# Performance work log

Hardware: AMD Instinct MI355X
Metric: run time of the kernel (lower is better)

Reference implementation:

```python
import jax, jax.numpy as jnp
import numpy as np

B, S, K, N = 4, 2048, 4096, 11008
GROUP_SIZE = 128
NUM_GROUPS = K // GROUP_SIZE  # 32


def setup_inputs() -> dict:
    key = jax.random.key(0)
    k1, k2, k3, k4, k5 = jax.random.split(key, 5)
    x = jax.random.normal(k1, (B, S, K), dtype=jnp.float32)
    # sensitivity-sorted column order is a permutation of [0, K)
    col_indices = jax.random.permutation(k2, K).astype(jnp.int32)
    # packed uint8 nibbles stored as int32 in [0, 256)
    w_packed = jax.random.randint(k3, (K // 2, N), 0, 256, dtype=jnp.int32)
    # per-group, per-output-column dequant scales (positive, small)
    scales = (jax.random.uniform(k4, (NUM_GROUPS, N), dtype=jnp.float32) + 0.05) * 0.01
    bias = jax.random.normal(k5, (N,), dtype=jnp.float32) * 0.01
    return {"x": x, "col_indices": col_indices, "w_packed": w_packed,
            "scales": scales, "bias": bias}


def _dequant_weight(w_packed, scales):
    # unpack int4 nibbles: low nibble -> even k, high nibble -> odd k
    low = (w_packed & 15) - 8          # [K//2, N]
    high = ((w_packed >> 4) & 15) - 8  # [K//2, N]
    w_int = jnp.stack([low, high], axis=1).reshape(K, N)  # interleaved [K, N]
    # per-group dequant: scale index = k // group_size
    w = w_int.astype(scales.dtype).reshape(NUM_GROUPS, GROUP_SIZE, N)
    w = w * scales[:, None, :]
    return w.reshape(K, N)


def reference(x, col_indices, w_packed, scales, bias):
    orig_shape = x.shape
    xm = x.reshape(-1, K)                     # [M, K]
    xg = jnp.take(xm, col_indices, axis=1)    # column-reorder gather [M, K]
    w = _dequant_weight(w_packed, scales)     # [K, N]
    out = jnp.einsum('mk,kn->mn', xg, w)      # fp32 accumulate
    out = out + bias
    return out.reshape(orig_shape[0], orig_shape[1], N)
```

## Files before the change

kernel.cpp:

```cpp
#include <hip/hip_runtime.h>
#include <hip/hip_bf16.h>
#include <stdint.h>

#define M_DIM 8192
#define K_DIM 4096
#define N_DIM 11008
#define NT32  128

typedef __attribute__((ext_vector_type(8))) short bf16x8;
typedef __attribute__((ext_vector_type(4))) float f32x4;
typedef __attribute__((ext_vector_type(4))) unsigned int uint4v;

__device__ __forceinline__ unsigned short f2bf(float f) {
    __hip_bfloat16 h = __float2bfloat16(f);
    return __builtin_bit_cast(unsigned short, h);
}

__device__ __forceinline__ void gload_lds16(const unsigned short* g, unsigned short* l) {
    __builtin_amdgcn_global_load_lds(
        (const __attribute__((address_space(1))) void*)g,
        (__attribute__((address_space(3))) void*)l,
        16, 0, 0);
}

__device__ __forceinline__ unsigned lds_addr(const unsigned short* p) {
    return (unsigned)(uintptr_t)(const __attribute__((address_space(3))) unsigned short*)p;
}

#define DSRI(dst, a, OFF) asm volatile("ds_read_b128 %0, %1 offset:%2" \
    : "=v"(dst) : "v"(a), "n"(OFF) : "memory")

#define LGKM(N) do { \
    asm volatile("s_waitcnt lgkmcnt(" #N ")" ::: "memory"); \
    __builtin_amdgcn_sched_barrier(0); \
} while (0)
#define BAR() do { __builtin_amdgcn_s_barrier(); asm volatile("" ::: "memory"); } while (0)

__global__ void permute_x_kernel(const float* __restrict__ x,
                                 const int* __restrict__ ci,
                                 unsigned short* __restrict__ xg) {
    int idx = blockIdx.x * 256 + threadIdx.x;
    int64_t base = (int64_t)idx * 4;
    int m = (int)(base >> 12);
    int k = (int)(base & 4095);
    const float* xrow = x + ((int64_t)m << 12);
    int4 c4 = *reinterpret_cast<const int4*>(ci + k);
    ushort4 o;
    o.x = f2bf(xrow[c4.x]);
    o.y = f2bf(xrow[c4.y]);
    o.z = f2bf(xrow[c4.z]);
    o.w = f2bf(xrow[c4.w]);
    *reinterpret_cast<ushort4*>(xg + base) = o;
}

__global__ void dequant_w_kernel(const int* __restrict__ wp,
                                 const float* __restrict__ scales,
                                 unsigned short* __restrict__ wT) {
    __shared__ unsigned short tile[64][65];
    int n0 = blockIdx.x * 64;
    int k0 = blockIdx.y * 64;
    int g = k0 >> 7;
    int t = threadIdx.x;
    int col = t & 63;
    int r0 = t >> 6;
    float s = scales[(int64_t)g * N_DIM + n0 + col];
    int pr0 = k0 >> 1;
#pragma unroll
    for (int i = 0; i < 8; ++i) {
        int row = r0 + i * 4;
        int p = wp[(int64_t)(pr0 + row) * N_DIM + n0 + col];
        tile[2 * row][col]     = f2bf((float)((p & 15) - 8) * s);
        tile[2 * row + 1][col] = f2bf((float)(((p >> 4) & 15) - 8) * s);
    }
    __syncthreads();
    int nl = t >> 2;
    int kk0 = (t & 3) << 4;
    unsigned short vals[16];
#pragma unroll
    for (int j = 0; j < 16; ++j) vals[j] = tile[kk0 + j][nl];
    uint4v* dst = reinterpret_cast<uint4v*>(wT + (int64_t)(n0 + nl) * K_DIM + k0 + kk0);
    dst[0] = *reinterpret_cast<const uint4v*>(&vals[0]);
    dst[1] = *reinterpret_cast<const uint4v*>(&vals[8]);
}


template <int BUF>
__device__ __forceinline__ void read_RA(bf16x8 (&a)[4], bf16x8 (&b)[4],
                                        unsigned aA01, unsigned aA2,
                                        unsigned bB01, unsigned bB2) {
    const unsigned ad = (BUF < 2) ? aA01 : aA2;
    const unsigned bd = (BUF < 2) ? bB01 : bB2;
    constexpr int bo = (BUF < 2) ? BUF * 32768 : 0;
    DSRI(a[0], ad, bo + 0);
    DSRI(a[1], ad, bo + 1024);
    DSRI(a[2], ad, bo + 2048);
    DSRI(a[3], ad, bo + 3072);
    DSRI(b[0], bd, bo + 0);
    DSRI(b[1], bd, bo + 1024);
    DSRI(b[2], bd, bo + 2048);
    DSRI(b[3], bd, bo + 3072);
}

template <int BUF>
__device__ __forceinline__ void read_RB(bf16x8 (&a2)[4], unsigned aA01, unsigned aA2) {
    const unsigned ad = (BUF < 2) ? aA01 : aA2;
    constexpr int bo = (BUF < 2) ? BUF * 32768 : 0;
    DSRI(a2[0], ad, bo + 4096);
    DSRI(a2[1], ad, bo + 5120);
    DSRI(a2[2], ad, bo + 6144);
    DSRI(a2[3], ad, bo + 7168);
}

template <int MB>
__device__ __forceinline__ void mfma4(f32x4 (&acc)[8][4], const bf16x8 (&av)[4],
                                      const bf16x8 (&bv)[4]) {
    __builtin_amdgcn_s_setprio(1);
#pragma unroll
    for (int m = 0; m < 4; ++m)
#pragma unroll
        for (int n = 0; n < 4; ++n)
            acc[MB + m][n] = __builtin_amdgcn_mfma_f32_16x16x32_bf16(
                av[m], bv[n], acc[MB + m][n], 0, 0, 0);
    __builtin_amdgcn_s_setprio(0);
}

template <int DBUF, int ISB>
__device__ __forceinline__ void stage2(const unsigned short* p0, const unsigned short* p1,
                                       int t, unsigned short* lds, int wLds) {
    const unsigned short* s0 = p0 + t * 32;
    const unsigned short* s1 = p1 + t * 32;
    unsigned short* d = lds + DBUF * 16384 + ISB * 8192 + wLds;
    gload_lds16(s0, d);
    gload_lds16(s1, d + 512);
}

#define PH_TILE(B, BN, BS, CA_, CB_, NA_, NB_, tt)                        \
    do {                                                                  \
        read_RB<B>(a2, aA01, aA2);                                        \
        stage2<BS, 0>(pA0, pA1, (tt), lds, wLds);                         \
        LGKM(4);                                                          \
        mfma4<0>(acc, CA_, CB_);                                          \
        asm volatile("s_waitcnt vmcnt(2)" ::: "memory");                  \
        BAR();                                                            \
        read_RA<BN>(NA_, NB_, aA01, aA2, bB01, bB2);                      \
        stage2<BS, 1>(pB0, pB1, (tt), lds, wLds);                         \
        LGKM(8);                                                          \
        mfma4<4>(acc, a2, CB_);                                           \
        BAR();                                                            \
    } while (0)

__global__ __launch_bounds__(512, 2)
void gemm_kernel(const unsigned short* __restrict__ A,
                 const unsigned short* __restrict__ BT,
                 const float* __restrict__ bias,
                 float* __restrict__ C) {
    __shared__ unsigned short lds[49152];

    constexpr int NT = N_DIM / 256;
    int wg = blockIdx.x, nwg = gridDim.x;
    int q = nwg >> 3, r = nwg & 7;
    int xcd = wg & 7, li = wg >> 3;
    int swz = (xcd < r ? xcd * (q + 1) : r * (q + 1) + (xcd - r) * q) + li;
    int by = swz / NT, bx = swz - by * NT;
    int brow = by << 8, bcol = bx << 8;

    int t = threadIdx.x;
    int lane = t & 63, w = t >> 6;
    int wr = w >> 2, wc = w & 3;
    int fr = lane & 15, fq = lane >> 4;

    const unsigned xr = (unsigned)((fr & 6) << 3);
    const int riw = lane >> 2;
    const int s8 = ((lane & 3) ^ ((lane >> 3) & 3)) << 3;
    const int w32 = w * 32, wLds = w * 1024;

    const unsigned ldsB = lds_addr(lds);
    const unsigned aA01 = ldsB + ((unsigned)((wr * 128 + fr) * 64 + fq * 16) ^ xr);
    const unsigned bB01 = ldsB + 16384u + ((unsigned)((wc * 64 + fr) * 64 + fq * 16) ^ xr);
    const unsigned aA2 = aA01 + 65536;
    const unsigned bB2 = bB01 + 65536;

    const unsigned short* pA0 = A + (int64_t)(brow + w32 + riw) * K_DIM + s8;
    const unsigned short* pA1 = pA0 + 16 * K_DIM;
    const unsigned short* pB0 = BT + (int64_t)(bcol + w32 + riw) * K_DIM + s8;
    const unsigned short* pB1 = pB0 + 16 * K_DIM;

    f32x4 acc[8][4];
#pragma unroll
    for (int m = 0; m < 8; ++m)
#pragma unroll
        for (int n = 0; n < 4; ++n) acc[m][n] = (f32x4){0.f, 0.f, 0.f, 0.f};

    bf16x8 aX[4], bX[4], aY[4], bY[4], a2[4];

    stage2<0, 0>(pA0, pA1, 0, lds, wLds);
    stage2<0, 1>(pB0, pB1, 0, lds, wLds);
    stage2<1, 0>(pA0, pA1, 1, lds, wLds);
    stage2<1, 1>(pB0, pB1, 1, lds, wLds);
    asm volatile("s_waitcnt vmcnt(4)" ::: "memory");
    BAR();
    read_RA<0>(aX, bX, aA01, aA2, bB01, bB2);

#pragma unroll 1
    for (int body = 0; body < 21; ++body) {
        const int t2 = body * 6 + 2;
        PH_TILE(0, 1, 2, aX, bX, aY, bY, t2);
        PH_TILE(1, 2, 0, aY, bY, aX, bX, t2 + 1);
        PH_TILE(2, 0, 1, aX, bX, aY, bY, t2 + 2);
        PH_TILE(0, 1, 2, aY, bY, aX, bX, t2 + 3);
        PH_TILE(1, 2, 0, aX, bX, aY, bY, t2 + 4);
        PH_TILE(2, 0, 1, aY, bY, aX, bX, t2 + 5);
    }

    read_RB<0>(a2, aA01, aA2);
    LGKM(4);
    mfma4<0>(acc, aX, bX);
    asm volatile("s_waitcnt vmcnt(0)" ::: "memory");
    BAR();
    read_RA<1>(aY, bY, aA01, aA2, bB01, bB2);
    LGKM(8);
    mfma4<4>(acc, a2, bX);
    BAR();
    read_RB<1>(a2, aA01, aA2);
    LGKM(4);
    mfma4<0>(acc, aY, bY);
    LGKM(0);
    mfma4<4>(acc, a2, bY);

    int orow0 = brow + wr * 128 + fq * 4;
    int ocol0 = bcol + wc * 64 + fr;
#pragma unroll
    for (int n = 0; n < 4; ++n) {
        int col = ocol0 + n * 16;
        float bval = bias[col];
#pragma unroll
        for (int m = 0; m < 8; ++m) {
            int row = orow0 + m * 16;
            float* cp = C + (int64_t)row * N_DIM + col;
#pragma unroll
            for (int j = 0; j < 4; ++j) {
                cp[(int64_t)j * N_DIM] = acc[m][n][j] + bval;
            }
        }
    }
}

extern "C" void kernel_launch(void* const* d_in, const int* in_sizes, int n_in,
                              void* d_out, int out_size, void* d_ws, size_t ws_size,
                              hipStream_t stream) {
    const float* x      = (const float*)d_in[0];
    const int* ci       = (const int*)d_in[1];
    const int* wp       = (const int*)d_in[2];
    const float* scales = (const float*)d_in[3];
    const float* bias   = (const float*)d_in[4];
    float* out          = (float*)d_out;

    const size_t wT_bytes = (size_t)N_DIM * K_DIM * 2;
    unsigned short* wT = (unsigned short*)d_ws;
    unsigned short* xg = wT + (size_t)N_DIM * K_DIM;

    size_t cap = (ws_size > wT_bytes) ? (ws_size - wT_bytes) : 0;
    int max_rows = (int)(cap / ((size_t)K_DIM * 2));
    int chunk_rows = (max_rows / 256) * 256;
    if (chunk_rows <= 0) chunk_rows = 256;
    if (chunk_rows > M_DIM) chunk_rows = M_DIM;

    dequant_w_kernel<<<dim3(N_DIM / 64, K_DIM / 64), 256, 0, stream>>>(wp, scales, wT);

    for (int m0 = 0; m0 < M_DIM; m0 += chunk_rows) {
        int rows = M_DIM - m0 < chunk_rows ? M_DIM - m0 : chunk_rows;
        int pgrid = (int)(((int64_t)rows * K_DIM) / (4 * 256));
        permute_x_kernel<<<pgrid, 256, 0, stream>>>(
            x + (int64_t)m0 * K_DIM, ci, xg);
        int grid = (rows / 256) * (N_DIM / 256);
        gemm_kernel<<<grid, 512, 0, stream>>>(
            xg, wT, bias, out + (int64_t)m0 * N_DIM);
    }
}
```

Before: 833.7 us.

## Switch GEMM inner loop from 16x16x32 to 32x32x16 bf16 MFMA tiles

Replaces the 16x16x32 MFMA micro-tiling (8x4 accumulators of 4 floats) with 32x32x16 MFMA (4x2 accumulators of 16 floats), and restructures the LDS reads into two K-halves per 64-wide stage. Each wave now issues fewer, larger MFMAs and reads fewer B fragments per tile, which lowers LDS read traffic and instruction count per FLOP. The LDS addressing, XOR swizzle and output indexing are rewritten to match the 32x32 register layout. The risk is bank conflicts from the new access pattern, and a less coalesced epilogue store pattern.

```diff
diff --git a/kernel.cpp b/kernel.cpp
--- a/kernel.cpp
+++ b/kernel.cpp
@@ -5,10 +5,10 @@
 #define M_DIM 8192
 #define K_DIM 4096
 #define N_DIM 11008
-#define NT32  128
 
 typedef __attribute__((ext_vector_type(8))) short bf16x8;
 typedef __attribute__((ext_vector_type(4))) float f32x4;
+typedef __attribute__((ext_vector_type(16))) float f32x16;
 typedef __attribute__((ext_vector_type(4))) unsigned int uint4v;
 
 __device__ __forceinline__ unsigned short f2bf(float f) {
@@ -84,44 +84,31 @@
 }
 
 
+__device__ __forceinline__ void mfma_tile(f32x16 (&acc)[4][2], const bf16x8 (&av)[4],
+                                          const bf16x8 (&bv)[2]) {
+    __builtin_amdgcn_s_setprio(1);
+#pragma unroll
+    for (int m = 0; m < 4; ++m)
+#pragma unroll
+        for (int n = 0; n < 2; ++n)
+            acc[m][n] = __builtin_amdgcn_mfma_f32_32x32x16_bf16(
+                av[m], bv[n], acc[m][n], 0, 0, 0);
+    __builtin_amdgcn_s_setprio(0);
+}
+
 template <int BUF>
-__device__ __forceinline__ void read_RA(bf16x8 (&a)[4], bf16x8 (&b)[4],
-                                        unsigned aA01, unsigned aA2,
-                                        unsigned bB01, unsigned bB2) {
-    const unsigned ad = (BUF < 2) ? aA01 : aA2;
-    const unsigned bd = (BUF < 2) ? bB01 : bB2;
+__device__ __forceinline__ void read_set(bf16x8 (&a)[4], bf16x8 (&b)[2],
+                                         unsigned aB, unsigned aB2,
+                                         unsigned bB, unsigned bB2) {
+    const unsigned ad = (BUF < 2) ? aB : aB2;
+    const unsigned bd = (BUF < 2) ? bB : bB2;
     constexpr int bo = (BUF < 2) ? BUF * 32768 : 0;
     DSRI(a[0], ad, bo + 0);
-    DSRI(a[1], ad, bo + 1024);
-    DSRI(a[2], ad, bo + 2048);
-    DSRI(a[3], ad, bo + 3072);
+    DSRI(a[1], ad, bo + 2048);
+    DSRI(a[2], ad, bo + 4096);
+    DSRI(a[3], ad, bo + 6144);
     DSRI(b[0], bd, bo + 0);
-    DSRI(b[1], bd, bo + 1024);
-    DSRI(b[2], bd, bo + 2048);
-    DSRI(b[3], bd, bo + 3072);
-}
-
-template <int BUF>
-__device__ __forceinline__ void read_RB(bf16x8 (&a2)[4], unsigned aA01, unsigned aA2) {
-    const unsigned ad = (BUF < 2) ? aA01 : aA2;
-    constexpr int bo = (BUF < 2) ? BUF * 32768 : 0;
-    DSRI(a2[0], ad, bo + 4096);
-    DSRI(a2[1], ad, bo + 5120);
-    DSRI(a2[2], ad, bo + 6144);
-    DSRI(a2[3], ad, bo + 7168);
-}
-
-template <int MB>
-__device__ __forceinline__ void mfma4(f32x4 (&acc)[8][4], const bf16x8 (&av)[4],
-                                      const bf16x8 (&bv)[4]) {
-    __builtin_amdgcn_s_setprio(1);
-#pragma unroll
-    for (int m = 0; m < 4; ++m)
-#pragma unroll
-        for (int n = 0; n < 4; ++n)
-            acc[MB + m][n] = __builtin_amdgcn_mfma_f32_16x16x32_bf16(
-                av[m], bv[n], acc[MB + m][n], 0, 0, 0);
-    __builtin_amdgcn_s_setprio(0);
+    DSRI(b[1], bd, bo + 2048);
 }
 
 template <int DBUF, int ISB>
@@ -136,16 +123,16 @@
 
 #define PH_TILE(B, BN, BS, CA_, CB_, NA_, NB_, tt)                        \
     do {                                                                  \
-        read_RB<B>(a2, aA01, aA2);                                        \
+        read_set<B>(aZ, bZ, aK1, aK1_2, bK1, bK1_2);                      \
         stage2<BS, 0>(pA0, pA1, (tt), lds, wLds);                         \
-        LGKM(4);                                                          \
-        mfma4<0>(acc, CA_, CB_);                                          \
+        LGKM(6);                                                          \
+        mfma_tile(acc, CA_, CB_);                                         \
         asm volatile("s_waitcnt vmcnt(2)" ::: "memory");                  \
         BAR();                                                            \
-        read_RA<BN>(NA_, NB_, aA01, aA2, bB01, bB2);                      \
+        read_set<BN>(NA_, NB_, aK0, aK0_2, bK0, bK0_2);                   \
         stage2<BS, 1>(pB0, pB1, (tt), lds, wLds);                         \
-        LGKM(8);                                                          \
-        mfma4<4>(acc, a2, CB_);                                           \
+        LGKM(6);                                                          \
+        mfma_tile(acc, aZ, bZ);                                           \
         BAR();                                                            \
     } while (0)
 
@@ -167,31 +154,37 @@
     int t = threadIdx.x;
     int lane = t & 63, w = t >> 6;
     int wr = w >> 2, wc = w & 3;
-    int fr = lane & 15, fq = lane >> 4;
-
-    const unsigned xr = (unsigned)((fr & 6) << 3);
+    int l31 = lane & 31, hi = lane >> 5;
+
+    const unsigned xr = (unsigned)((lane & 6) << 3);
     const int riw = lane >> 2;
     const int s8 = ((lane & 3) ^ ((lane >> 3) & 3)) << 3;
     const int w32 = w * 32, wLds = w * 1024;
 
     const unsigned ldsB = lds_addr(lds);
-    const unsigned aA01 = ldsB + ((unsigned)((wr * 128 + fr) * 64 + fq * 16) ^ xr);
-    const unsigned bB01 = ldsB + 16384u + ((unsigned)((wc * 64 + fr) * 64 + fq * 16) ^ xr);
-    const unsigned aA2 = aA01 + 65536;
-    const unsigned bB2 = bB01 + 65536;
+    const unsigned lin_a = (unsigned)((wr * 128 + l31) * 64 + hi * 16);
+    const unsigned lin_b = (unsigned)((wc * 64 + l31) * 64 + hi * 16);
+    const unsigned aK0 = ldsB + (lin_a ^ xr);
+    const unsigned aK1 = ldsB + ((lin_a + 32) ^ xr);
+    const unsigned bK0 = ldsB + 16384u + (lin_b ^ xr);
+    const unsigned bK1 = ldsB + 16384u + ((lin_b + 32) ^ xr);
+    const unsigned aK0_2 = aK0 + 65536, aK1_2 = aK1 + 65536;
+    const unsigned bK0_2 = bK0 + 65536, bK1_2 = bK1 + 65536;
 
     const unsigned short* pA0 = A + (int64_t)(brow + w32 + riw) * K_DIM + s8;
     const unsigned short* pA1 = pA0 + 16 * K_DIM;
     const unsigned short* pB0 = BT + (int64_t)(bcol + w32 + riw) * K_DIM + s8;
     const unsigned short* pB1 = pB0 + 16 * K_DIM;
 
-    f32x4 acc[8][4];
-#pragma unroll
-    for (int m = 0; m < 8; ++m)
-#pragma unroll
-        for (int n = 0; n < 4; ++n) acc[m][n] = (f32x4){0.f, 0.f, 0.f, 0.f};
-
-    bf16x8 aX[4], bX[4], aY[4], bY[4], a2[4];
+    f32x16 acc[4][2];
+#pragma unroll
+    for (int m = 0; m < 4; ++m)
+#pragma unroll
+        for (int n = 0; n < 2; ++n)
+#pragma unroll
+            for (int j = 0; j < 16; ++j) acc[m][n][j] = 0.f;
+
+    bf16x8 aX[4], bX[2], aY[4], bY[2], aZ[4], bZ[2];
 
     stage2<0, 0>(pA0, pA1, 0, lds, wLds);
     stage2<0, 1>(pB0, pB1, 0, lds, wLds);
@@ -199,7 +192,7 @@
     stage2<1, 1>(pB0, pB1, 1, lds, wLds);
     asm volatile("s_waitcnt vmcnt(4)" ::: "memory");
     BAR();
-    read_RA<0>(aX, bX, aA01, aA2, bB01, bB2);
+    read_set<0>(aX, bX, aK0, aK0_2, bK0, bK0_2);
 
 #pragma unroll 1
     for (int body = 0; body < 21; ++body) {
@@ -212,34 +205,34 @@
         PH_TILE(2, 0, 1, aY, bY, aX, bX, t2 + 5);
     }
 
-    read_RB<0>(a2, aA01, aA2);
-    LGKM(4);
-    mfma4<0>(acc, aX, bX);
+    read_set<0>(aZ, bZ, aK1, aK1_2, bK1, bK1_2);
+    LGKM(6);
+    mfma_tile(acc, aX, bX);
     asm volatile("s_waitcnt vmcnt(0)" ::: "memory");
     BAR();
-    read_RA<1>(aY, bY, aA01, aA2, bB01, bB2);
-    LGKM(8);
-    mfma4<4>(acc, a2, bX);
+    read_set<1>(aY, bY, aK0, aK0_2, bK0, bK0_2);
+    LGKM(6);
+    mfma_tile(acc, aZ, bZ);
     BAR();
-    read_RB<1>(a2, aA01, aA2);
-    LGKM(4);
-    mfma4<0>(acc, aY, bY);
+    read_set<1>(aZ, bZ, aK1, aK1_2, bK1, bK1_2);
+    LGKM(6);
+    mfma_tile(acc, aY, bY);
     LGKM(0);
-    mfma4<4>(acc, a2, bY);
-
-    int orow0 = brow + wr * 128 + fq * 4;
-    int ocol0 = bcol + wc * 64 + fr;
-#pragma unroll
-    for (int n = 0; n < 4; ++n) {
-        int col = ocol0 + n * 16;
+    mfma_tile(acc, aZ, bZ);
+
+    int orow0 = brow + wr * 128 + 4 * hi;
+    int ocol0 = bcol + wc * 64 + l31;
+#pragma unroll
+    for (int n = 0; n < 2; ++n) {
+        int col = ocol0 + n * 32;
         float bval = bias[col];
 #pragma unroll
-        for (int m = 0; m < 8; ++m) {
-            int row = orow0 + m * 16;
-            float* cp = C + (int64_t)row * N_DIM + col;
-#pragma unroll
-            for (int j = 0; j < 4; ++j) {
-                cp[(int64_t)j * N_DIM] = acc[m][n][j] + bval;
+        for (int m = 0; m < 4; ++m) {
+            int rbase = orow0 + m * 32;
+#pragma unroll
+            for (int j = 0; j < 16; ++j) {
+                int row = rbase + (j & 3) + 8 * (j >> 2);
+                C[(int64_t)row * N_DIM + col] = acc[m][n][j] + bval;
             }
         }
     }
```

After: 838.8 us. Within noise of the previous version (+0.6%).

## Deepen GEMM LDS pipeline from triple to quad buffering and drop setprio

Applied to the files above, without the earlier changes.

Grows shared memory from three to four K-stage buffers (128KB) so global-to-LDS prefetch runs three tiles ahead, and relaxes vmcnt waits accordingly. The main loop is re-unrolled over four buffers, with a peeled tail handling the last tiles. It also removes the s_setprio around the MFMA blocks. The larger LDS footprint may limit occupancy to one workgroup per CU despite launch_bounds(512,2), which could offset the extra latency hiding.

```diff
diff --git a/kernel.cpp b/kernel.cpp
--- a/kernel.cpp
+++ b/kernel.cpp
@@ -5,7 +5,6 @@
 #define M_DIM 8192
 #define K_DIM 4096
 #define N_DIM 11008
-#define NT32  128
 
 typedef __attribute__((ext_vector_type(8))) short bf16x8;
 typedef __attribute__((ext_vector_type(4))) float f32x4;
@@ -34,6 +33,7 @@
     asm volatile("s_waitcnt lgkmcnt(" #N ")" ::: "memory"); \
     __builtin_amdgcn_sched_barrier(0); \
 } while (0)
+#define VMC(N) asm volatile("s_waitcnt vmcnt(" #N ")" ::: "memory")
 #define BAR() do { __builtin_amdgcn_s_barrier(); asm volatile("" ::: "memory"); } while (0)
 
 __global__ void permute_x_kernel(const float* __restrict__ x,
@@ -86,11 +86,11 @@
 
 template <int BUF>
 __device__ __forceinline__ void read_RA(bf16x8 (&a)[4], bf16x8 (&b)[4],
-                                        unsigned aA01, unsigned aA2,
-                                        unsigned bB01, unsigned bB2) {
-    const unsigned ad = (BUF < 2) ? aA01 : aA2;
-    const unsigned bd = (BUF < 2) ? bB01 : bB2;
-    constexpr int bo = (BUF < 2) ? BUF * 32768 : 0;
+                                        unsigned aA01, unsigned aA23,
+                                        unsigned bB01, unsigned bB23) {
+    const unsigned ad = (BUF < 2) ? aA01 : aA23;
+    const unsigned bd = (BUF < 2) ? bB01 : bB23;
+    constexpr int bo = (BUF & 1) * 32768;
     DSRI(a[0], ad, bo + 0);
     DSRI(a[1], ad, bo + 1024);
     DSRI(a[2], ad, bo + 2048);
@@ -102,9 +102,9 @@
 }
 
 template <int BUF>
-__device__ __forceinline__ void read_RB(bf16x8 (&a2)[4], unsigned aA01, unsigned aA2) {
-    const unsigned ad = (BUF < 2) ? aA01 : aA2;
-    constexpr int bo = (BUF < 2) ? BUF * 32768 : 0;
+__device__ __forceinline__ void read_RB(bf16x8 (&a2)[4], unsigned aA01, unsigned aA23) {
+    const unsigned ad = (BUF < 2) ? aA01 : aA23;
+    constexpr int bo = (BUF & 1) * 32768;
     DSRI(a2[0], ad, bo + 4096);
     DSRI(a2[1], ad, bo + 5120);
     DSRI(a2[2], ad, bo + 6144);
@@ -114,14 +114,12 @@
 template <int MB>
 __device__ __forceinline__ void mfma4(f32x4 (&acc)[8][4], const bf16x8 (&av)[4],
                                       const bf16x8 (&bv)[4]) {
-    __builtin_amdgcn_s_setprio(1);
 #pragma unroll
     for (int m = 0; m < 4; ++m)
 #pragma unroll
         for (int n = 0; n < 4; ++n)
             acc[MB + m][n] = __builtin_amdgcn_mfma_f32_16x16x32_bf16(
                 av[m], bv[n], acc[MB + m][n], 0, 0, 0);
-    __builtin_amdgcn_s_setprio(0);
 }
 
 template <int DBUF, int ISB>
@@ -136,13 +134,13 @@
 
 #define PH_TILE(B, BN, BS, CA_, CB_, NA_, NB_, tt)                        \
     do {                                                                  \
-        read_RB<B>(a2, aA01, aA2);                                        \
+        read_RB<B>(a2, aA01, aA23);                                       \
         stage2<BS, 0>(pA0, pA1, (tt), lds, wLds);                         \
         LGKM(4);                                                          \
         mfma4<0>(acc, CA_, CB_);                                          \
-        asm volatile("s_waitcnt vmcnt(2)" ::: "memory");                  \
+        VMC(6);                                                           \
         BAR();                                                            \
-        read_RA<BN>(NA_, NB_, aA01, aA2, bB01, bB2);                      \
+        read_RA<BN>(NA_, NB_, aA01, aA23, bB01, bB23);                    \
         stage2<BS, 1>(pB0, pB1, (tt), lds, wLds);                         \
         LGKM(8);                                                          \
         mfma4<4>(acc, a2, CB_);                                           \
@@ -154,7 +152,7 @@
                  const unsigned short* __restrict__ BT,
                  const float* __restrict__ bias,
                  float* __restrict__ C) {
-    __shared__ unsigned short lds[49152];
+    __shared__ unsigned short lds[65536];
 
     constexpr int NT = N_DIM / 256;
     int wg = blockIdx.x, nwg = gridDim.x;
@@ -177,8 +175,8 @@
     const unsigned ldsB = lds_addr(lds);
     const unsigned aA01 = ldsB + ((unsigned)((wr * 128 + fr) * 64 + fq * 16) ^ xr);
     const unsigned bB01 = ldsB + 16384u + ((unsigned)((wc * 64 + fr) * 64 + fq * 16) ^ xr);
-    const unsigned aA2 = aA01 + 65536;
-    const unsigned bB2 = bB01 + 65536;
+    const unsigned aA23 = aA01 + 65536;
+    const unsigned bB23 = bB01 + 65536;
 
     const unsigned short* pA0 = A + (int64_t)(brow + w32 + riw) * K_DIM + s8;
     const unsigned short* pA1 = pA0 + 16 * K_DIM;
@@ -197,31 +195,41 @@
     stage2<0, 1>(pB0, pB1, 0, lds, wLds);
     stage2<1, 0>(pA0, pA1, 1, lds, wLds);
     stage2<1, 1>(pB0, pB1, 1, lds, wLds);
-    asm volatile("s_waitcnt vmcnt(4)" ::: "memory");
-    BAR();
-    read_RA<0>(aX, bX, aA01, aA2, bB01, bB2);
+    stage2<2, 0>(pA0, pA1, 2, lds, wLds);
+    stage2<2, 1>(pB0, pB1, 2, lds, wLds);
+    VMC(8);
+    BAR();
+    read_RA<0>(aX, bX, aA01, aA23, bB01, bB23);
 
 #pragma unroll 1
-    for (int body = 0; body < 21; ++body) {
-        const int t2 = body * 6 + 2;
-        PH_TILE(0, 1, 2, aX, bX, aY, bY, t2);
-        PH_TILE(1, 2, 0, aY, bY, aX, bX, t2 + 1);
-        PH_TILE(2, 0, 1, aX, bX, aY, bY, t2 + 2);
-        PH_TILE(0, 1, 2, aY, bY, aX, bX, t2 + 3);
-        PH_TILE(1, 2, 0, aX, bX, aY, bY, t2 + 4);
-        PH_TILE(2, 0, 1, aY, bY, aX, bX, t2 + 5);
-    }
-
-    read_RB<0>(a2, aA01, aA2);
+    for (int body = 0; body < 31; ++body) {
+        const int t3 = body * 4 + 3;
+        PH_TILE(0, 1, 3, aX, bX, aY, bY, t3);
+        PH_TILE(1, 2, 0, aY, bY, aX, bX, t3 + 1);
+        PH_TILE(2, 3, 1, aX, bX, aY, bY, t3 + 2);
+        PH_TILE(3, 0, 2, aY, bY, aX, bX, t3 + 3);
+    }
+
+    PH_TILE(0, 1, 3, aX, bX, aY, bY, 127);
+    read_RB<1>(a2, aA01, aA23);
+    LGKM(4);
+    mfma4<0>(acc, aY, bY);
+    VMC(4);
+    BAR();
+    read_RA<2>(aX, bX, aA01, aA23, bB01, bB23);
+    LGKM(8);
+    mfma4<4>(acc, a2, bY);
+    BAR();
+    read_RB<2>(a2, aA01, aA23);
     LGKM(4);
     mfma4<0>(acc, aX, bX);
-    asm volatile("s_waitcnt vmcnt(0)" ::: "memory");
-    BAR();
-    read_RA<1>(aY, bY, aA01, aA2, bB01, bB2);
+    VMC(0);
+    BAR();
+    read_RA<3>(aY, bY, aA01, aA23, bB01, bB23);
     LGKM(8);
     mfma4<4>(acc, a2, bX);
     BAR();
-    read_RB<1>(a2, aA01, aA2);
+    read_RB<3>(a2, aA01, aA23);
     LGKM(4);
     mfma4<0>(acc, aY, bY);
     LGKM(0);
```

New measurement: 813.7 us. 1.02x faster.
